# Optimization experiments

Measured on AMD Instinct MI355X. Metric: run time of the kernel, lower is better.

## Reference

```python
import jax, jax.numpy as jnp
import numpy as np

NOPEN = 64
NNIN = 16
NUM_OUTPUT = 64
NLAYER = 4
H = 0.1
TF = 1.0
N_NODES = 50000
N_EDGES = 1600000


def setup_inputs() -> dict:
    key = jax.random.key(0)
    k1, k2, k3, k4, k5, k6 = jax.random.split(key, 6)
    xn = jax.random.normal(k1, (1, NNIN, N_NODES), dtype=jnp.float32)
    iInd = jax.random.randint(k2, (N_EDGES,), 0, N_NODES)
    jInd = jax.random.randint(k3, (N_EDGES,), 0, N_NODES)
    # learned parameters per original init
    K1Nopen = jax.random.normal(k4, (NOPEN, NNIN), dtype=jnp.float32) * 0.01
    KN1 = jnp.eye(NOPEN, dtype=jnp.float32) + jax.random.uniform(k5, (NOPEN, NOPEN), dtype=jnp.float32) * 0.001
    KNclose = jax.random.normal(k6, (NUM_OUTPUT, NOPEN), dtype=jnp.float32) * 0.01
    return {"xn": xn, "iInd": iInd, "jInd": jInd, "n_nodes": N_NODES,
            "K1Nopen": K1Nopen, "KN1": KN1, "KNclose": KNclose}


def _gcn_norm(I, J, n_nodes, dtype):
    # add self-loops, symmetric normalization deg^{-1/2}[row]*deg^{-1/2}[col]
    loops = jnp.arange(n_nodes, dtype=I.dtype)
    I2 = jnp.concatenate([I, loops])
    J2 = jnp.concatenate([J, loops])
    ew = jnp.ones(I2.shape[0], dtype=dtype)
    deg = jax.ops.segment_sum(ew, J2, num_segments=n_nodes)
    dinv = jnp.where(deg > 0, 1.0 / jnp.sqrt(deg), 0.0)
    w = dinv[I2] * dinv[J2]
    return I2, J2, w


def reference(xn, iInd, jInd, n_nodes, K1Nopen, KN1, KNclose):
    I, J, w = _gcn_norm(iInd, jInd, n_nodes, xn.dtype)  # [E+N]

    # OpenFlatLayer: 1x1 conv1d with K1Nopen + relu (openclose=True, norm=False)
    x = jax.nn.relu(jnp.einsum('oi,bin->bon', K1Nopen, xn))  # [1, nopen, N]

    dt = TF / NLAYER
    wb = w[None, None, :]
    for _ in range(NLAYER):
        # nodeGrad: edge features [1, nopen, E]
        g = wb * (x[:, :, I] - x[:, :, J])
        # singleLayer (openclose=False): conv(K), relu, conv(K.t())
        z = jax.nn.relu(jnp.einsum('oi,bie->boe', KN1, g))
        z = jnp.einsum('io,bie->boe', KN1, z)
        # edgeDiv: scatter-add w*z at I minus at J
        wz = jnp.moveaxis(wb * z, -1, 0)  # [E, 1, nopen]
        div = (jax.ops.segment_sum(wz, I, num_segments=n_nodes)
               - jax.ops.segment_sum(wz, J, num_segments=n_nodes))
        div = jnp.moveaxis(div, 0, -1)  # [1, nopen, N]
        # forward Euler: step layer returns -h*div, integrated with dt
        x = x - dt * H * div

    # CloseLayer: 1x1 conv1d, squeeze().t(), log_softmax over channels
    xc = jnp.einsum('oi,bin->bon', KNclose, x)[0].T  # [N, num_output]
    return jax.nn.log_softmax(xc, axis=1)
```

## Files before the change

kernel.cpp:

```cpp
#include <hip/hip_runtime.h>

#define NN 50000
#define NE 1600000
#define C 64
#define NIN 16
#define DTH 0.025f
#define ASC 16.0f
#define USC 64.0f
#define SDIV 16384.0f
#define SLOT 128

#define NB2 256
#define NPB 196
#define CAP 16384
#define ABLK 1024
#define EPB 1563
#define RND 2048
#define BINC 32
#define GSTR 16
#define OPEN_GRID 1024

typedef _Float16 f16x2 __attribute__((ext_vector_type(2)));
typedef float f32x2 __attribute__((ext_vector_type(2)));
union U32H2 { uint32_t u; f16x2 h; };

#define RL(x, l) __int_as_float(__builtin_amdgcn_readlane(__float_as_int(x), (l)))

__global__ void k_setup(const float* __restrict__ KN1, const float* __restrict__ KNc,
                        float* __restrict__ M2s, float* __restrict__ KMs,
                        int* __restrict__ gcur) {
    if (threadIdx.x < NB2) gcur[threadIdx.x * GSTR] = 0;
    for (int idx = threadIdx.x; idx < C * C; idx += blockDim.x) {
        int p = idx >> 6, o = idx & 63;
        float s1 = 0.f, s2 = 0.f;
        for (int i = 0; i < C; i++) {
            s1 = fmaf(KN1[o * C + i], KN1[p * C + i], s1);
            s2 = fmaf(KNc[o * C + i], KN1[p * C + i], s2);
        }
        M2s[idx] = s1;
        KMs[idx] = s2;
    }
}

__launch_bounds__(256)
__global__ void k_binA(const int* __restrict__ iInd, const int* __restrict__ jInd,
                       int* __restrict__ gcur, uint32_t* __restrict__ stg) {
    __shared__ uint32_t bins[NB2][BINC];
    __shared__ int bcnt[NB2];
    __shared__ int gbase[NB2];
    int tid = threadIdx.x;
    int eBeg = blockIdx.x * EPB;
    int eEnd = eBeg + EPB; if (eEnd > NE) eEnd = NE;
    for (int rb = eBeg; rb < eEnd; rb += RND) {
        for (int b = tid; b < NB2; b += 256) bcnt[b] = 0;
        __syncthreads();
        int rEnd = rb + RND; if (rEnd > eEnd) rEnd = eEnd;
        for (int e = rb + tid; e < rEnd; e += 256) {
            int i = __builtin_nontemporal_load(&iInd[e]);
            int j = __builtin_nontemporal_load(&jInd[e]);
            {
                int b = (unsigned)i / NPB;
                uint32_t ent = ((unsigned)(i - b * NPB) << 17) | (unsigned)j;
                int pos = atomicAdd(&bcnt[b], 1);
                if (pos < BINC) bins[b][pos] = ent;
                else { int gp = atomicAdd(&gcur[b * GSTR], 1);
                       if (gp < CAP) stg[(size_t)b * CAP + gp] = ent; }
            }
            {
                int b = (unsigned)j / NPB;
                uint32_t ent = ((unsigned)(j - b * NPB) << 17) | 0x10000u | (unsigned)i;
                int pos = atomicAdd(&bcnt[b], 1);
                if (pos < BINC) bins[b][pos] = ent;
                else { int gp = atomicAdd(&gcur[b * GSTR], 1);
                       if (gp < CAP) stg[(size_t)b * CAP + gp] = ent; }
            }
        }
        __syncthreads();
        {
            int c = bcnt[tid]; if (c > BINC) c = BINC;
            gbase[tid] = (c > 0) ? atomicAdd(&gcur[tid * GSTR], c) : 0;
        }
        __syncthreads();
        for (int idx = tid; idx < NB2 * BINC; idx += 256) {
            int b = idx >> 5, k = idx & (BINC - 1);
            int c = bcnt[b]; if (c > BINC) c = BINC;
            if (k < c) {
                int pos = gbase[b] + k;
                if (pos < CAP) stg[(size_t)b * CAP + pos] = bins[b][k];
            }
        }
        __syncthreads();
    }
}

#define LADJ (NPB * SLOT)
__launch_bounds__(1024)
__global__ void k_binB(const int* __restrict__ gcur, const uint32_t* __restrict__ stg,
                       unsigned* __restrict__ pk, float* __restrict__ dinv,
                       uint32_t* __restrict__ adjp) {
    __shared__ unsigned lcnt[NPB];
    __shared__ uint32_t ladj[LADJ];
    int b = blockIdx.x, tid = threadIdx.x;
    if (tid < NPB) lcnt[tid] = 0;
    __syncthreads();
    int cnt = gcur[b * GSTR]; if (cnt > CAP) cnt = CAP;
    int n0 = b * NPB;
    for (int k = tid; k < cnt; k += 1024) {
        uint32_t ent = stg[(size_t)b * CAP + k];
        int tl = (int)(ent >> 17);
        unsigned sign = (ent >> 16) & 1u;
        unsigned other = ent & 0xFFFFu;
        unsigned ret = atomicAdd(&lcnt[tl], 1u + (sign << 16));
        unsigned slot = ret & 0xFFFFu;
        if (slot < SLOT) ladj[(tl << 7) + slot] = other | (sign << 31);
    }
    __syncthreads();
    if (tid < NPB) {
        int n = n0 + tid;
        if (n < NN) {
            unsigned v = lcnt[tid];
            unsigned c = v & 0xFFFFu; if (c > SLOT) c = SLOT;
            unsigned deg = (v >> 16) + 1u;
            pk[n] = (deg << 16) | c;
            dinv[n] = 1.0f / sqrtf((float)deg);
        }
    }
    int nval = NN - n0; if (nval > NPB) nval = NPB; if (nval < 0) nval = 0;
    int totv = (nval << 7) >> 2;
    uint4* gdst = (uint4*)(adjp + ((size_t)n0 << 7));
    const uint4* lsrc = (const uint4*)ladj;
    for (int v = tid; v < totv; v += 1024) gdst[v] = lsrc[v];
}

__global__ void k_weight(const unsigned* __restrict__ pk, const float* __restrict__ dinv,
                         uint32_t* __restrict__ adjp) {
    int idx = blockIdx.x * 256 + threadIdx.x;
    int n = idx >> 7, p = idx & (SLOT - 1);
    int cnt = (int)(pk[n] & 0xFFFFu); if (cnt > SLOT) cnt = SLOT;
    int pad = (cnt + 31) & ~31;
    if (p < cnt) {
        uint32_t e = adjp[idx];
        int other = (int)(e & 0xFFFFu);
        float a = ASC * dinv[n] * dinv[other];
        float w = 0.5f * a * a;
        if (e >> 31) w = -w;
        U32H2 t; t.u = (unsigned)other; t.h.y = (_Float16)w;
        adjp[idx] = t.u;
    } else if (p < pad) {
        adjp[idx] = 0u;
    }
}

static __device__ __forceinline__ void store_u8(uint32_t* __restrict__ u8, int n, int lane, float su) {
    float v1 = __shfl_down(su, 1, 64);
    float v2 = __shfl_down(su, 2, 64);
    float v3 = __shfl_down(su, 3, 64);
    if ((lane & 3) == 0) {
        int p0 = __builtin_amdgcn_cvt_pk_fp8_f32(su, v1, 0, false);
        int p1 = __builtin_amdgcn_cvt_pk_fp8_f32(v2, v3, p0, true);
        u8[n * 16 + (lane >> 2)] = (uint32_t)p1;
    }
}

__launch_bounds__(512)
__global__ void k_open_u(const float* __restrict__ xn, const float* __restrict__ K1,
                         const float* __restrict__ KN1, const float* __restrict__ KNc,
                         _Float16* __restrict__ u0, uint32_t* __restrict__ u8,
                         float* __restrict__ co) {
    __shared__ float sK1[NIN * C];
    __shared__ float sU[C * C];
    __shared__ float sC[C * C];
    for (int idx = threadIdx.x; idx < NIN * C; idx += 512) {
        int i = idx >> 6, o = idx & 63;
        sK1[idx] = K1[o * NIN + i];
    }
    for (int idx = threadIdx.x; idx < C * C; idx += 512) {
        int o = idx >> 6, p = idx & 63;
        int sw = (o << 6) | (p ^ ((o & 7) << 2));
        sU[sw] = KN1[idx];
        sC[sw] = KNc[idx];
    }
    __syncthreads();
    int wv = threadIdx.x >> 6, lane = threadIdx.x & 63;
    int mb = lane << 6, lx = (lane & 7) << 2;
    for (int pr = blockIdx.x * 8 + wv; pr < NN / 2; pr += OPEN_GRID * 8) {
        int nA = pr * 2, nB = nA + 1;
        float xA = 0.f, xB = 0.f;
#pragma unroll
        for (int i = 0; i < NIN; i++) {
            float k1 = sK1[i * C + lane];
            xA = fmaf(k1, xn[i * NN + nA], xA);
            xB = fmaf(k1, xn[i * NN + nB], xB);
        }
        xA = fmaxf(xA, 0.f); xB = fmaxf(xB, 0.f);
        float uA0 = 0.f, uA1 = 0.f, uB0 = 0.f, uB1 = 0.f;
        float cA0 = 0.f, cA1 = 0.f, cB0 = 0.f, cB1 = 0.f;
#pragma unroll
        for (int p0 = 0; p0 < C; p0 += 4) {
            const float4 mu = *(const float4*)&sU[mb + (p0 ^ lx)];
            const float4 mc = *(const float4*)&sC[mb + (p0 ^ lx)];
            float a0 = RL(xA, p0 + 0), a1 = RL(xA, p0 + 1);
            float a2 = RL(xA, p0 + 2), a3 = RL(xA, p0 + 3);
            float b0 = RL(xB, p0 + 0), b1 = RL(xB, p0 + 1);
            float b2 = RL(xB, p0 + 2), b3 = RL(xB, p0 + 3);
            uA0 = fmaf(mu.x, a0, uA0); uA1 = fmaf(mu.y, a1, uA1);
            uA0 = fmaf(mu.z, a2, uA0); uA1 = fmaf(mu.w, a3, uA1);
            uB0 = fmaf(mu.x, b0, uB0); uB1 = fmaf(mu.y, b1, uB1);
            uB0 = fmaf(mu.z, b2, uB0); uB1 = fmaf(mu.w, b3, uB1);
            cA0 = fmaf(mc.x, a0, cA0); cA1 = fmaf(mc.y, a1, cA1);
            cA0 = fmaf(mc.z, a2, cA0); cA1 = fmaf(mc.w, a3, cA1);
            cB0 = fmaf(mc.x, b0, cB0); cB1 = fmaf(mc.y, b1, cB1);
            cB0 = fmaf(mc.z, b2, cB0); cB1 = fmaf(mc.w, b3, cB1);
        }
        float uA = uA0 + uA1, uB = uB0 + uB1;
        u0[(size_t)nA * C + lane] = (_Float16)uA;
        u0[(size_t)nB * C + lane] = (_Float16)uB;
        store_u8(u8, nA, lane, uA * USC);
        store_u8(u8, nB, lane, uB * USC);
        co[(size_t)nA * C + lane] = cA0 + cA1;
        co[(size_t)nB * C + lane] = cB0 + cB1;
    }
}

#define ACCR(WW, QQ, A0, A1, A2, A3, U0, U1, U2, U3) {                        \
    U32H2 aw; aw.u = (WW);                                                    \
    float w_ = (float)aw.h.y;                                                 \
    f32x2 lo_ = __builtin_amdgcn_cvt_pk_f32_fp8((int)(QQ), false);            \
    f32x2 hi_ = __builtin_amdgcn_cvt_pk_f32_fp8((int)(QQ), true);             \
    float d0_ = (U0) - lo_.x, d1_ = (U1) - lo_.y;                             \
    float d2_ = (U2) - hi_.x, d3_ = (U3) - hi_.y;                             \
    A0 = fmaf(w_, __builtin_fabsf(d0_), fmaf(__builtin_fabsf(w_), d0_, A0));  \
    A1 = fmaf(w_, __builtin_fabsf(d1_), fmaf(__builtin_fabsf(w_), d1_, A1));  \
    A2 = fmaf(w_, __builtin_fabsf(d2_), fmaf(__builtin_fabsf(w_), d2_, A2));  \
    A3 = fmaf(w_, __builtin_fabsf(d3_), fmaf(__builtin_fabsf(w_), d3_, A3));  \
}

#define GATHER2_BODY(PKA, ADJP, U8R)                                          \
    uint32_t unqA = (U8R)[nA * 16 + li];                                      \
    uint32_t unqB = (U8R)[nB * 16 + li];                                      \
    f32x2 alo = __builtin_amdgcn_cvt_pk_f32_fp8((int)unqA, false);            \
    f32x2 ahi = __builtin_amdgcn_cvt_pk_f32_fp8((int)unqA, true);             \
    f32x2 blo = __builtin_amdgcn_cvt_pk_f32_fp8((int)unqB, false);            \
    f32x2 bhi = __builtin_amdgcn_cvt_pk_f32_fp8((int)unqB, true);             \
    float uA0 = alo.x, uA1 = alo.y, uA2 = ahi.x, uA3 = ahi.y;                 \
    float uB0 = blo.x, uB1 = blo.y, uB2 = bhi.x, uB3 = bhi.y;                 \
    uint2 pk2_ = *(const uint2*)&(PKA)[nA];                                   \
    int degA = (int)(pk2_.x & 0xFFFFu); if (degA > SLOT) degA = SLOT;         \
    int degB = (int)(pk2_.y & 0xFFFFu); if (degB > SLOT) degB = SLOT;         \
    int padA = (degA + 31) & ~31, padB = (degB + 31) & ~31;                   \
    int baseA = nA << 7, baseB = nB << 7;                                     \
    int maxPad = padA > padB ? padA : padB;                                   \
    float aA0 = 0.f, aA1 = 0.f, aA2 = 0.f, aA3 = 0.f;                         \
    float aB0 = 0.f, aB1 = 0.f, aB2 = 0.f, aB3 = 0.f;                         \
    for (int c0 = 0; c0 < maxPad; c0 += 32) {                                 \
        uint32_t wA[8], qA[8], wB[8], qB[8];                                  \
        bool dA = c0 < padA, dB = c0 < padB;                                  \
        if (dA) {                                                             \
            _Pragma("unroll")                                                 \
            for (int r = 0; r < 8; r++) wA[r] = (ADJP)[baseA + c0 + r * 4 + g]; \
        }                                                                     \
        if (dB) {                                                             \
            _Pragma("unroll")                                                 \
            for (int r = 0; r < 8; r++) wB[r] = (ADJP)[baseB + c0 + r * 4 + g]; \
        }                                                                     \
        if (dA) {                                                             \
            _Pragma("unroll")                                                 \
            for (int r = 0; r < 8; r++) qA[r] = (U8R)[(wA[r] & 0xFFFFu) * 16 + li]; \
        }                                                                     \
        if (dB) {                                                             \
            _Pragma("unroll")                                                 \
            for (int r = 0; r < 8; r++) qB[r] = (U8R)[(wB[r] & 0xFFFFu) * 16 + li]; \
        }                                                                     \
        if (dA) {                                                             \
            _Pragma("unroll")                                                 \
            for (int r = 0; r < 8; r++) ACCR(wA[r], qA[r], aA0, aA1, aA2, aA3, uA0, uA1, uA2, uA3) \
        }                                                                     \
        if (dB) {                                                             \
            _Pragma("unroll")                                                 \
            for (int r = 0; r < 8; r++) ACCR(wB[r], qB[r], aB0, aB1, aB2, aB3, uB0, uB1, uB2, uB3) \
        }                                                                     \
    }                                                                         \
    aA0 += __shfl_xor(aA0, 16, 64); aA0 += __shfl_xor(aA0, 32, 64);           \
    aA1 += __shfl_xor(aA1, 16, 64); aA1 += __shfl_xor(aA1, 32, 64);           \
    aA2 += __shfl_xor(aA2, 16, 64); aA2 += __shfl_xor(aA2, 32, 64);           \
    aA3 += __shfl_xor(aA3, 16, 64); aA3 += __shfl_xor(aA3, 32, 64);           \
    aB0 += __shfl_xor(aB0, 16, 64); aB0 += __shfl_xor(aB0, 32, 64);           \
    aB1 += __shfl_xor(aB1, 16, 64); aB1 += __shfl_xor(aB1, 32, 64);           \
    aB2 += __shfl_xor(aB2, 16, 64); aB2 += __shfl_xor(aB2, 32, 64);           \
    aB3 += __shfl_xor(aB3, 16, 64); aB3 += __shfl_xor(aB3, 32, 64);           \
    float rA0 = __shfl(aA0, lane >> 2, 64), rA1 = __shfl(aA1, lane >> 2, 64); \
    float rA2 = __shfl(aA2, lane >> 2, 64), rA3 = __shfl(aA3, lane >> 2, 64); \
    float rB0 = __shfl(aB0, lane >> 2, 64), rB1 = __shfl(aB1, lane >> 2, 64); \
    float rB2 = __shfl(aB2, lane >> 2, 64), rB3 = __shfl(aB3, lane >> 2, 64); \
    float sA_lane = (lane & 2) ? ((lane & 1) ? rA3 : rA2)                     \
                               : ((lane & 1) ? rA1 : rA0);                    \
    float sB_lane = (lane & 2) ? ((lane & 1) ? rB3 : rB2)                     \
                               : ((lane & 1) ? rB1 : rB0);

#define STAGE_MT(SMT, SRC) {                                                  \
    for (int idx = threadIdx.x; idx < C * C; idx += 256) {                    \
        int p_ = idx >> 6, c_ = idx & 63;                                     \
        (SMT)[(c_ << 6) | (p_ ^ ((c_ & 7) << 2))] = (SRC)[idx];               \
    }                                                                         \
}

#define MATVEC2(SMT, SAV, SBV, DUA, DUB) {                                    \
    float mA0_ = 0.f, mA1_ = 0.f, mB0_ = 0.f, mB1_ = 0.f;                     \
    int mb_ = (lane << 6), lx_ = (lane & 7) << 2;                             \
    _Pragma("unroll")                                                         \
    for (int p0 = 0; p0 < 64; p0 += 4) {                                      \
        const float4 mv = *(const float4*)&(SMT)[mb_ + (p0 ^ lx_)];           \
        mA0_ = fmaf(mv.x, RL(SAV, p0 + 0), mA0_);                             \
        mA1_ = fmaf(mv.y, RL(SAV, p0 + 1), mA1_);                             \
        mA0_ = fmaf(mv.z, RL(SAV, p0 + 2), mA0_);                             \
        mA1_ = fmaf(mv.w, RL(SAV, p0 + 3), mA1_);                             \
        mB0_ = fmaf(mv.x, RL(SBV, p0 + 0), mB0_);                             \
        mB1_ = fmaf(mv.y, RL(SBV, p0 + 1), mB1_);                             \
        mB0_ = fmaf(mv.z, RL(SBV, p0 + 2), mB0_);                             \
        mB1_ = fmaf(mv.w, RL(SBV, p0 + 3), mB1_);                             \
    }                                                                         \
    DUA = mA0_ + mA1_; DUB = mB0_ + mB1_;                                     \
}

__launch_bounds__(256, 8)
__global__ void k_gather_upd(const unsigned* __restrict__ pk, const uint32_t* __restrict__ adjp,
                             const uint32_t* __restrict__ u8r, const _Float16* __restrict__ ucur,
                             const float* __restrict__ M2s, float* __restrict__ sacc,
                             _Float16* __restrict__ unext, uint32_t* __restrict__ u8w, int beta) {
    __shared__ float sMt[C * C];
    STAGE_MT(sMt, M2s)
    __syncthreads();
    int wv = threadIdx.x >> 6, lane = threadIdx.x & 63;
    int g = lane >> 4, li = lane & 15;
    int nA = (blockIdx.x * 4 + wv) * 2;
    int nB = nA + 1;
    GATHER2_BODY(pk, adjp, u8r)
    float duA, duB;
    MATVEC2(sMt, sA_lane, sB_lane, duA, duB)
    float unewA = (float)ucur[(size_t)nA * C + lane] - (DTH / SDIV) * duA;
    float unewB = (float)ucur[(size_t)nB * C + lane] - (DTH / SDIV) * duB;
    unext[(size_t)nA * C + lane] = (_Float16)unewA;
    unext[(size_t)nB * C + lane] = (_Float16)unewB;
    store_u8(u8w, nA, lane, unewA * USC);
    store_u8(u8w, nB, lane, unewB * USC);
    size_t ixA = (size_t)nA * C + lane, ixB = (size_t)nB * C + lane;
    sacc[ixA] = beta ? (sacc[ixA] + sA_lane) : sA_lane;
    sacc[ixB] = beta ? (sacc[ixB] + sB_lane) : sB_lane;
}

__launch_bounds__(256, 8)
__global__ void k_gather_close(const unsigned* __restrict__ pk, const uint32_t* __restrict__ adjp,
                               const uint32_t* __restrict__ u8r, const float* __restrict__ KMs,
                               const float* __restrict__ sacc, const float* __restrict__ co,
                               float* __restrict__ out) {
    __shared__ float sKMt[C * C];
    STAGE_MT(sKMt, KMs)
    __syncthreads();
    int wv = threadIdx.x >> 6, lane = threadIdx.x & 63;
    int g = lane >> 4, li = lane & 15;
    int nA = (blockIdx.x * 4 + wv) * 2;
    int nB = nA + 1;
    GATHER2_BODY(pk, adjp, u8r)
    float stotA = sA_lane + sacc[(size_t)nA * C + lane];
    float stotB = sB_lane + sacc[(size_t)nB * C + lane];
    float dxA, dxB;
    MATVEC2(sKMt, stotA, stotB, dxA, dxB)
    float oA = co[(size_t)nA * C + lane] - (DTH / SDIV) * dxA;
    float oB = co[(size_t)nB * C + lane] - (DTH / SDIV) * dxB;
    float mA = oA, mB = oB;
#pragma unroll
    for (int off2 = 32; off2; off2 >>= 1) {
        mA = fmaxf(mA, __shfl_xor(mA, off2, 64));
        mB = fmaxf(mB, __shfl_xor(mB, off2, 64));
    }
    float sumA = expf(oA - mA), sumB = expf(oB - mB);
#pragma unroll
    for (int off2 = 32; off2; off2 >>= 1) {
        sumA += __shfl_xor(sumA, off2, 64);
        sumB += __shfl_xor(sumB, off2, 64);
    }
    out[(size_t)nA * C + lane] = oA - mA - logf(sumA);
    out[(size_t)nB * C + lane] = oB - mB - logf(sumB);
}

extern "C" void kernel_launch(void* const* d_in, const int* in_sizes, int n_in,
                              void* d_out, int out_size, void* d_ws, size_t ws_size,
                              hipStream_t stream) {
    (void)in_sizes; (void)n_in; (void)out_size; (void)ws_size;
    const float* xn   = (const float*)d_in[0];
    const int* iInd   = (const int*)d_in[1];
    const int* jInd   = (const int*)d_in[2];
    const float* K1   = (const float*)d_in[4];
    const float* KN1  = (const float*)d_in[5];
    const float* KNc  = (const float*)d_in[6];
    float* out = (float*)d_out;

    char* base = (char*)d_ws;
    size_t off = 0;
    auto alloc = [&](size_t bytes) { char* p = base + off; off = (off + bytes + 255) & ~(size_t)255; return p; };
    float* M2s  = (float*)alloc(C * C * 4);
    float* KMs  = (float*)alloc(C * C * 4);
    int* gcur   = (int*)alloc(NB2 * GSTR * 4);
    unsigned* pk = (unsigned*)alloc(NN * 4);
    float* dinv = (float*)alloc(NN * 4);
    float* co   = (float*)alloc((size_t)NN * C * 4);
    float* sacc = (float*)alloc((size_t)NN * C * 4);
    _Float16* ua = (_Float16*)alloc((size_t)NN * C * 2);
    _Float16* ub = (_Float16*)alloc((size_t)NN * C * 2);
    uint32_t* u8a = (uint32_t*)alloc((size_t)NN * 16 * 4);
    uint32_t* u8b = (uint32_t*)alloc((size_t)NN * 16 * 4);
    uint32_t* stg = (uint32_t*)alloc((size_t)NB2 * CAP * 4);
    uint32_t* adjp = (uint32_t*)alloc((size_t)NN * SLOT * 4);

    k_setup<<<1, 256, 0, stream>>>(KN1, KNc, M2s, KMs, gcur);
    k_binA<<<ABLK, 256, 0, stream>>>(iInd, jInd, gcur, stg);
    k_binB<<<NB2, 1024, 0, stream>>>(gcur, stg, pk, dinv, adjp);
    k_weight<<<(NN * SLOT) / 256, 256, 0, stream>>>(pk, dinv, adjp);

    k_open_u<<<OPEN_GRID, 512, 0, stream>>>(xn, K1, KN1, KNc, ua, u8a, co);

    const int GB = NN / 8;
    k_gather_upd<<<GB, 256, 0, stream>>>(pk, adjp, u8a, ua, M2s, sacc, ub, u8b, 0);
    k_gather_upd<<<GB, 256, 0, stream>>>(pk, adjp, u8b, ub, M2s, sacc, ua, u8a, 1);
    k_gather_upd<<<GB, 256, 0, stream>>>(pk, adjp, u8a, ua, M2s, sacc, ub, u8b, 1);
    k_gather_close<<<GB, 256, 0, stream>>>(pk, adjp, u8b, KMs, sacc, co, out);
}
```

Before: 508.2 us.

## Rewrite open layer as one-node-per-lane kernel with LDS transpose for stores

Replaces the wave-per-node-pair open kernel, which used readlane broadcasts and LDS-resident weights, with a kernel where each lane owns one node. Each lane computes all 64 channels in registers, reading weights through uniform (scalar) loads, then transposes through padded LDS so it can write vectorized fp16, fp8 and fp32 outputs. The kernel is also launched before the binning kernels. The cost targeted is readlane and LDS overhead; in exchange it uses many more registers per thread, and with 196 blocks of 256 threads the GPU may be underfilled.

Result: slower. 544.9 us (+7.2%).

```diff
diff --git a/kernel.cpp b/kernel.cpp
--- a/kernel.cpp
+++ b/kernel.cpp
@@ -18,7 +18,7 @@
 #define RND 2048
 #define BINC 32
 #define GSTR 16
-#define OPEN_GRID 1024
+#define OBLK 196
 
 typedef _Float16 f16x2 __attribute__((ext_vector_type(2)));
 typedef float f32x2 __attribute__((ext_vector_type(2)));
@@ -39,6 +39,85 @@
         }
         M2s[idx] = s1;
         KMs[idx] = s2;
+    }
+}
+
+__launch_bounds__(256)
+__global__ void k_open(const float* __restrict__ xn, const float* __restrict__ K1,
+                       const float* __restrict__ KN1, const float* __restrict__ KNc,
+                       _Float16* __restrict__ u0, uint32_t* __restrict__ u8,
+                       float* __restrict__ co) {
+    __shared__ float sbuf[4][C * 65];
+    int wv = threadIdx.x >> 6, lane = threadIdx.x & 63;
+    int nb = (blockIdx.x * 4 + wv) * 64;
+    int n = nb + lane;
+    int nc = n < NN ? n : NN - 1;
+    float* lf = sbuf[wv];
+
+    float xi[NIN];
+#pragma unroll
+    for (int i = 0; i < NIN; i++) xi[i] = xn[i * NN + nc];
+
+    float x[C];
+#pragma unroll
+    for (int p = 0; p < C; p++) {
+        float a = 0.f;
+#pragma unroll
+        for (int i = 0; i < NIN; i++) a = fmaf(K1[p * NIN + i], xi[i], a);
+        x[p] = fmaxf(a, 0.f);
+    }
+
+    for (int o = 0; o < C; o++) {
+        float a0 = 0.f, a1 = 0.f, a2 = 0.f, a3 = 0.f;
+#pragma unroll
+        for (int p = 0; p < C; p += 4) {
+            a0 = fmaf(KN1[o * C + p + 0], x[p + 0], a0);
+            a1 = fmaf(KN1[o * C + p + 1], x[p + 1], a1);
+            a2 = fmaf(KN1[o * C + p + 2], x[p + 2], a2);
+            a3 = fmaf(KN1[o * C + p + 3], x[p + 3], a3);
+        }
+        lf[o * 65 + lane] = (a0 + a1) + (a2 + a3);
+    }
+    for (int r = 0; r < 16; r++) {
+        int k = r * 4 + (lane >> 4);
+        int c0 = (lane & 15) * 4;
+        float f0 = lf[(c0 + 0) * 65 + k];
+        float f1 = lf[(c0 + 1) * 65 + k];
+        float f2 = lf[(c0 + 2) * 65 + k];
+        float f3 = lf[(c0 + 3) * 65 + k];
+        int nk = nb + k;
+        if (nk < NN) {
+            union { uint32_t w[2]; _Float16 h[4]; } t;
+            t.h[0] = (_Float16)f0; t.h[1] = (_Float16)f1;
+            t.h[2] = (_Float16)f2; t.h[3] = (_Float16)f3;
+            *(uint2*)&u0[(size_t)nk * C + c0] = make_uint2(t.w[0], t.w[1]);
+            int p0 = __builtin_amdgcn_cvt_pk_fp8_f32(f0 * USC, f1 * USC, 0, false);
+            int p1 = __builtin_amdgcn_cvt_pk_fp8_f32(f2 * USC, f3 * USC, p0, true);
+            u8[nk * 16 + (c0 >> 2)] = (uint32_t)p1;
+        }
+    }
+
+    for (int o = 0; o < C; o++) {
+        float a0 = 0.f, a1 = 0.f, a2 = 0.f, a3 = 0.f;
+#pragma unroll
+        for (int p = 0; p < C; p += 4) {
+            a0 = fmaf(KNc[o * C + p + 0], x[p + 0], a0);
+            a1 = fmaf(KNc[o * C + p + 1], x[p + 1], a1);
+            a2 = fmaf(KNc[o * C + p + 2], x[p + 2], a2);
+            a3 = fmaf(KNc[o * C + p + 3], x[p + 3], a3);
+        }
+        lf[o * 65 + lane] = (a0 + a1) + (a2 + a3);
+    }
+    for (int r = 0; r < 16; r++) {
+        int k = r * 4 + (lane >> 4);
+        int c0 = (lane & 15) * 4;
+        float4 v;
+        v.x = lf[(c0 + 0) * 65 + k];
+        v.y = lf[(c0 + 1) * 65 + k];
+        v.z = lf[(c0 + 2) * 65 + k];
+        v.w = lf[(c0 + 3) * 65 + k];
+        int nk = nb + k;
+        if (nk < NN) *(float4*)&co[(size_t)nk * C + c0] = v;
     }
 }
 
@@ -162,66 +241,6 @@
     }
 }
 
-__launch_bounds__(512)
-__global__ void k_open_u(const float* __restrict__ xn, const float* __restrict__ K1,
-                         const float* __restrict__ KN1, const float* __restrict__ KNc,
-                         _Float16* __restrict__ u0, uint32_t* __restrict__ u8,
-                         float* __restrict__ co) {
-    __shared__ float sK1[NIN * C];
-    __shared__ float sU[C * C];
-    __shared__ float sC[C * C];
-    for (int idx = threadIdx.x; idx < NIN * C; idx += 512) {
-        int i = idx >> 6, o = idx & 63;
-        sK1[idx] = K1[o * NIN + i];
-    }
-    for (int idx = threadIdx.x; idx < C * C; idx += 512) {
-        int o = idx >> 6, p = idx & 63;
-        int sw = (o << 6) | (p ^ ((o & 7) << 2));
-        sU[sw] = KN1[idx];
-        sC[sw] = KNc[idx];
-    }
-    __syncthreads();
-    int wv = threadIdx.x >> 6, lane = threadIdx.x & 63;
-    int mb = lane << 6, lx = (lane & 7) << 2;
-    for (int pr = blockIdx.x * 8 + wv; pr < NN / 2; pr += OPEN_GRID * 8) {
-        int nA = pr * 2, nB = nA + 1;
-        float xA = 0.f, xB = 0.f;
-#pragma unroll
-        for (int i = 0; i < NIN; i++) {
-            float k1 = sK1[i * C + lane];
-            xA = fmaf(k1, xn[i * NN + nA], xA);
-            xB = fmaf(k1, xn[i * NN + nB], xB);
-        }
-        xA = fmaxf(xA, 0.f); xB = fmaxf(xB, 0.f);
-        float uA0 = 0.f, uA1 = 0.f, uB0 = 0.f, uB1 = 0.f;
-        float cA0 = 0.f, cA1 = 0.f, cB0 = 0.f, cB1 = 0.f;
-#pragma unroll
-        for (int p0 = 0; p0 < C; p0 += 4) {
-            const float4 mu = *(const float4*)&sU[mb + (p0 ^ lx)];
-            const float4 mc = *(const float4*)&sC[mb + (p0 ^ lx)];
-            float a0 = RL(xA, p0 + 0), a1 = RL(xA, p0 + 1);
-            float a2 = RL(xA, p0 + 2), a3 = RL(xA, p0 + 3);
-            float b0 = RL(xB, p0 + 0), b1 = RL(xB, p0 + 1);
-            float b2 = RL(xB, p0 + 2), b3 = RL(xB, p0 + 3);
-            uA0 = fmaf(mu.x, a0, uA0); uA1 = fmaf(mu.y, a1, uA1);
-            uA0 = fmaf(mu.z, a2, uA0); uA1 = fmaf(mu.w, a3, uA1);
-            uB0 = fmaf(mu.x, b0, uB0); uB1 = fmaf(mu.y, b1, uB1);
-            uB0 = fmaf(mu.z, b2, uB0); uB1 = fmaf(mu.w, b3, uB1);
-            cA0 = fmaf(mc.x, a0, cA0); cA1 = fmaf(mc.y, a1, cA1);
-            cA0 = fmaf(mc.z, a2, cA0); cA1 = fmaf(mc.w, a3, cA1);
-            cB0 = fmaf(mc.x, b0, cB0); cB1 = fmaf(mc.y, b1, cB1);
-            cB0 = fmaf(mc.z, b2, cB0); cB1 = fmaf(mc.w, b3, cB1);
-        }
-        float uA = uA0 + uA1, uB = uB0 + uB1;
-        u0[(size_t)nA * C + lane] = (_Float16)uA;
-        u0[(size_t)nB * C + lane] = (_Float16)uB;
-        store_u8(u8, nA, lane, uA * USC);
-        store_u8(u8, nB, lane, uB * USC);
-        co[(size_t)nA * C + lane] = cA0 + cA1;
-        co[(size_t)nB * C + lane] = cB0 + cB1;
-    }
-}
-
 #define ACCR(WW, QQ, A0, A1, A2, A3, U0, U1, U2, U3) {                        \
     U32H2 aw; aw.u = (WW);                                                    \
     float w_ = (float)aw.h.y;                                                 \
@@ -413,11 +432,10 @@
     uint32_t* adjp = (uint32_t*)alloc((size_t)NN * SLOT * 4);
 
     k_setup<<<1, 256, 0, stream>>>(KN1, KNc, M2s, KMs, gcur);
+    k_open<<<OBLK, 256, 0, stream>>>(xn, K1, KN1, KNc, ua, u8a, co);
     k_binA<<<ABLK, 256, 0, stream>>>(iInd, jInd, gcur, stg);
     k_binB<<<NB2, 1024, 0, stream>>>(gcur, stg, pk, dinv, adjp);
     k_weight<<<(NN * SLOT) / 256, 256, 0, stream>>>(pk, dinv, adjp);
-
-    k_open_u<<<OPEN_GRID, 512, 0, stream>>>(xn, K1, KN1, KNc, ua, u8a, co);
 
     const int GB = NN / 8;
     k_gather_upd<<<GB, 256, 0, stream>>>(pk, adjp, u8a, ua, M2s, sacc, ub, u8b, 0);
```
